# Optimization experiments

Measured on AMD Instinct MI355X. Metric: run time of the kernel, lower is better.

## Reference

```python
import jax, jax.numpy as jnp
import numpy as np

B, SEQ, PRED, DM = 16, 2048, 2048, 64
P = SEQ + PRED            # PointNum = 4096, per-node feature length
NLAYER, HID = 3, 4096     # MLPNums, ggdmodel hidden sizes
NH, HS = 16, 4096         # NumAttentionHeads, HiddenSize
G_CONST, K = 1.0, 8
NN = DM * DM              # 4096 == P, MHSA input dim (required by original code)


def setup_inputs() -> dict:
    key = jax.random.key(0)
    ks = jax.random.split(key, 11)
    s_mlp = 1.0 / np.sqrt(P).astype(np.float32)
    s_att = 1.0 / np.sqrt(NN).astype(np.float32)
    s_out = 1.0 / np.sqrt(HS).astype(np.float32)
    return {
        "x": jax.random.normal(ks[0], (B, P, DM), jnp.float32),
        "W_mlp": jax.random.normal(ks[1], (NLAYER, P, HID), jnp.float32) * s_mlp,
        "b_mlp": jnp.zeros((NLAYER, HID), jnp.float32),
        "Wq": jax.random.normal(ks[2], (NN, HS), jnp.float32) * s_att,
        "bq": jnp.zeros((HS,), jnp.float32),
        "Wk": jax.random.normal(ks[3], (NN, HS), jnp.float32) * s_att,
        "bk": jnp.zeros((HS,), jnp.float32),
        "Wv": jax.random.normal(ks[4], (NN, HS), jnp.float32) * s_att,
        "bv": jnp.zeros((HS,), jnp.float32),
        "Wo": jax.random.normal(ks[5], (HS, HS), jnp.float32) * s_out,
        "bo": jnp.zeros((HS,), jnp.float32),
    }


def _grav_adj(h):
    # h: [B, N, D] node features -> symmetrized, top-K masked gravity adjacency [B, N, N]
    norm = jnp.linalg.norm(h, axis=-1)                      # [B, N]
    m = jnp.sum(h, axis=-1) / norm                          # node "mass"
    sim = jnp.einsum('bnd,bmd->bnm', h, h) / (norm[:, :, None] * norm[:, None, :])
    F = G_CONST * m[:, :, None] * m[:, None, :] * sim * sim  # gravity matrix
    kth = jax.lax.top_k(F, K)[0][..., -1:]                  # per-row Kth largest value
    F = jnp.where(F >= kth, F, 0.0)                         # keep only top-K per row
    F = jnp.maximum(F, 0.0)                                 # ReLU
    return 0.5 * (F + jnp.swapaxes(F, -1, -2))              # symmetrize


def reference(x, W_mlp, b_mlp, Wq, bq, Wk, bk, Wv, bv, Wo, bo):
    h = jnp.swapaxes(x, 1, 2)                               # [B, N=DM, P]
    adjs = [_grav_adj(h)]
    for l in range(NLAYER):                                 # each MLP applied to the same h
        hv = h @ W_mlp[l] + b_mlp[l]                        # [B, N, HID]
        adjs.append(_grav_adj(hv))
    A = jnp.stack(adjs, axis=1)                             # [B, L, N, N], L = NLAYER + 1
    Lseq = A.shape[1]
    tok = A.reshape(B, Lseq, NN)                            # L tokens of dim N*N
    dh = HS // NH
    q = (tok @ Wq + bq).reshape(B, Lseq, NH, dh)
    k = (tok @ Wk + bk).reshape(B, Lseq, NH, dh)
    v = (tok @ Wv + bv).reshape(B, Lseq, NH, dh)
    scores = jnp.einsum('blhd,bmhd->bhlm', q, k) / np.sqrt(dh).astype(np.float32)
    attn = jax.nn.softmax(scores, axis=-1)
    ctx = jnp.einsum('bhlm,bmhd->blhd', attn, v).reshape(B, Lseq, HS)
    out = ctx @ Wo + bo                                     # [B, L, HS]
    return jnp.where(out > 0.5, out, 0.0)
```

## Files before the change

### kernel.cpp

```cpp
#include <hip/hip_runtime.h>
#include <math.h>


#define B16 16
#define PDIM 4096
#define NNODE 64
#define NCHUNK 32
#define KCG 128

typedef __attribute__((ext_vector_type(8))) short bf16x8;
typedef __attribute__((ext_vector_type(4))) float f32x4;
typedef __attribute__((ext_vector_type(4))) unsigned short us4;
typedef __attribute__((ext_vector_type(8))) unsigned short us8;

__device__ inline void split2(float x, unsigned short& h, unsigned short& l) {
  unsigned u = __float_as_uint(x);
  unsigned hu = (u + 0x7fffu + ((u >> 16) & 1u)) & 0xffff0000u;
  h = (unsigned short)(hu >> 16);
  float lo = x - __uint_as_float(hu);
  unsigned u2 = __float_as_uint(lo);
  l = (unsigned short)((u2 + 0x7fffu + ((u2 >> 16) & 1u)) >> 16);
}

__device__ inline void gload16(const void* g, void* lds) {
  __builtin_amdgcn_global_load_lds((const unsigned int*)g, (unsigned int*)lds, 16, 0, 0);
}

__global__ __launch_bounds__(256) void k_transpose(const float* __restrict__ x,
                                                   float* __restrict__ h,
                                                   unsigned short* __restrict__ AhT,
                                                   unsigned short* __restrict__ AlT,
                                                   int do_split) {
  __shared__ float t[64][65];
  int b = blockIdx.y;
  int p0 = blockIdx.x * 64;
  const float* xb = x + (size_t)b * PDIM * NNODE;
  float* hb = h + (size_t)b * NNODE * PDIM;
#pragma unroll
  for (int i = 0; i < 16; ++i) {
    int e = i * 256 + threadIdx.x;
    int p = e >> 6, n = e & 63;
    t[p][n] = xb[(size_t)p0 * 64 + e];
  }
  __syncthreads();
#pragma unroll
  for (int i = 0; i < 16; ++i) {
    int e = i * 256 + threadIdx.x;
    int n = e >> 6, p = e & 63;
    hb[(size_t)n * PDIM + p0 + p] = t[p][n];
  }
  if (!do_split) return;
#pragma unroll
  for (int j = 0; j < 2; ++j) {
    int cid = j * 256 + threadIdx.x;
    int n2 = cid >> 3, kg8 = cid & 7;
    us8 hv_, lv_;
#pragma unroll
    for (int e = 0; e < 8; ++e) {
      unsigned short hh, ll;
      split2(t[kg8 * 8 + e][n2], hh, ll);
      hv_[e] = hh; lv_[e] = ll;
    }
    int m = b * 64 + n2;
    int ks = (p0 >> 5) + (kg8 >> 2);
    size_t idx = (((size_t)(m >> 7) * 128 + ks) * 8 + ((m >> 4) & 7)) * 512 +
                 (size_t)((n2 & 15) + 16 * (kg8 & 3)) * 8;
    *(us8*)&AhT[idx] = hv_;
    *(us8*)&AlT[idx] = lv_;
  }
}

__global__ __launch_bounds__(256) void k_wsplit(const float* __restrict__ W,
                                                unsigned short* __restrict__ WhT,
                                                unsigned short* __restrict__ WlT) {
  __shared__ float Wt[32][132];
  int nb = blockIdx.x, kb = blockIdx.y;
  int tid = threadIdx.x;
#pragma unroll
  for (int i = 0; i < 4; ++i) {
    int idx = i * 256 + tid;
    int row = idx >> 5, c4 = idx & 31;
    float4 v = *(const float4*)&W[(size_t)(kb * 32 + row) * 4096 + nb * 128 + c4 * 4];
    *(float4*)&Wt[row][c4 * 4] = v;
  }
  __syncthreads();
#pragma unroll
  for (int j = 0; j < 2; ++j) {
    int cid = j * 256 + tid;
    int nl = cid & 127, kg = cid >> 7;
    us8 hv_, lv_;
#pragma unroll
    for (int e = 0; e < 8; ++e) {
      unsigned short hh, ll;
      split2(Wt[kg * 8 + e][nl], hh, ll);
      hv_[e] = hh; lv_[e] = ll;
    }
    size_t idx = (((size_t)nb * 128 + kb) * 8 + (nl >> 4)) * 512 +
                 (size_t)((nl & 15) + 16 * kg) * 8;
    *(us8*)&WhT[idx] = hv_;
    *(us8*)&WlT[idx] = lv_;
  }
}

__global__ __launch_bounds__(512, 4) void k_gemm_bf16(
    const unsigned short* __restrict__ Ah, const unsigned short* __restrict__ Al,
    const unsigned short* __restrict__ Bh, const unsigned short* __restrict__ Bl,
    float* __restrict__ Cp, int Ksteps, int ksplit, int N, int mstore) {
  __shared__ unsigned short sAh[2][4096], sAl[2][4096];
  __shared__ unsigned short sBh[2][4096], sBl[2][4096];
  int tid = threadIdx.x;
  int l = tid & 63, wid = tid >> 6;
  int wr = wid >> 2, wc = wid & 3;
  int nb = blockIdx.x, mb = blockIdx.y, z = blockIdx.z;
  int spp = Ksteps / ksplit;
  int ks0 = z * spp;

  const size_t abase = ((size_t)mb * Ksteps + ks0) * 4096 + tid * 8;
  const size_t bbase = ((size_t)nb * Ksteps + ks0) * 4096 + tid * 8;

  f32x4 acc[4][2];
#pragma unroll
  for (int i = 0; i < 4; ++i)
#pragma unroll
    for (int j = 0; j < 2; ++j) acc[i][j] = (f32x4){0.f, 0.f, 0.f, 0.f};

  gload16(Ah + abase, &sAh[0][tid * 8]);
  gload16(Al + abase, &sAl[0][tid * 8]);
  gload16(Bh + bbase, &sBh[0][tid * 8]);
  gload16(Bl + bbase, &sBl[0][tid * 8]);
  __syncthreads();

  int buf = 0;
  for (int t = 0; t < spp; ++t) {
    if (t + 1 < spp) {
      size_t off = (size_t)(t + 1) * 4096;
      gload16(Ah + abase + off, &sAh[buf ^ 1][tid * 8]);
      gload16(Al + abase + off, &sAl[buf ^ 1][tid * 8]);
      gload16(Bh + bbase + off, &sBh[buf ^ 1][tid * 8]);
      gload16(Bl + bbase + off, &sBl[buf ^ 1][tid * 8]);
    }
    bf16x8 ah[4], al4[4], bh2[2], bl2[2];
#pragma unroll
    for (int mt = 0; mt < 4; ++mt) {
      ah[mt]  = *(const bf16x8*)&sAh[buf][(wr * 4 + mt) * 512 + l * 8];
      al4[mt] = *(const bf16x8*)&sAl[buf][(wr * 4 + mt) * 512 + l * 8];
    }
#pragma unroll
    for (int nt = 0; nt < 2; ++nt) {
      bh2[nt] = *(const bf16x8*)&sBh[buf][(wc * 2 + nt) * 512 + l * 8];
      bl2[nt] = *(const bf16x8*)&sBl[buf][(wc * 2 + nt) * 512 + l * 8];
    }
#pragma unroll
    for (int mt = 0; mt < 4; ++mt)
#pragma unroll
      for (int nt = 0; nt < 2; ++nt) {
        acc[mt][nt] = __builtin_amdgcn_mfma_f32_16x16x32_bf16(ah[mt],  bh2[nt], acc[mt][nt], 0, 0, 0);
        acc[mt][nt] = __builtin_amdgcn_mfma_f32_16x16x32_bf16(ah[mt],  bl2[nt], acc[mt][nt], 0, 0, 0);
        acc[mt][nt] = __builtin_amdgcn_mfma_f32_16x16x32_bf16(al4[mt], bh2[nt], acc[mt][nt], 0, 0, 0);
      }
    __syncthreads();
    buf ^= 1;
  }

  int n0 = nb * 128, m0 = mb * 128;
  float* Cz = Cp + (size_t)z * mstore * N;
#pragma unroll
  for (int mt = 0; mt < 4; ++mt)
#pragma unroll
    for (int nt = 0; nt < 2; ++nt) {
      int col = n0 + wc * 32 + nt * 16 + (l & 15);
#pragma unroll
      for (int r = 0; r < 4; ++r) {
        int row = m0 + wr * 64 + mt * 16 + ((l >> 4) << 2) + r;
        if (row < mstore) Cz[(size_t)row * N + col] = acc[mt][nt][r];
      }
    }
}

__global__ __launch_bounds__(256) void k_red_mlp(const float* __restrict__ Cp,
                                                 const float* __restrict__ bias,
                                                 float* __restrict__ hv) {
  int idx = blockIdx.x * 256 + threadIdx.x;
  hv[idx] = Cp[idx] + Cp[idx + 4194304] + bias[idx & 4095];
}

__global__ __launch_bounds__(256) void k_red16(const float* __restrict__ Cp,
                                               const float* __restrict__ bias,
                                               float* __restrict__ dst, int thr) {
  int idx = blockIdx.x * 256 + threadIdx.x;
  float s = bias[idx & 4095];
#pragma unroll
  for (int p = 0; p < 16; ++p) s += Cp[(size_t)p * 262144 + idx];
  if (thr) s = (s > 0.5f) ? s : 0.f;
  dst[idx] = s;
}

__global__ __launch_bounds__(256) void k_gram_partial(const float* __restrict__ Z,
                                                      float* __restrict__ Gp,
                                                      float* __restrict__ Sp) {
  __shared__ float Zt[KCG][68];
  int c = blockIdx.x, b = blockIdx.y;
  int tid = threadIdx.x;
  const float* Zb = Z + (size_t)b * NNODE * PDIM + c * KCG;
#pragma unroll
  for (int i = 0; i < 32; ++i) {
    int e = i * 256 + tid;
    int r = e >> 7, kk = e & 127;
    Zt[kk][r] = Zb[(size_t)r * PDIM + kk];
  }
  __syncthreads();
  int ii = tid >> 2, j0 = (tid & 3) << 4;
  float acc[16] = {};
  for (int kk = 0; kk < KCG; ++kk) {
    float zi = Zt[kk][ii];
    float4 z0 = *(const float4*)&Zt[kk][j0 + 0];
    float4 z1 = *(const float4*)&Zt[kk][j0 + 4];
    float4 z2 = *(const float4*)&Zt[kk][j0 + 8];
    float4 z3 = *(const float4*)&Zt[kk][j0 + 12];
    acc[0] = fmaf(zi, z0.x, acc[0]);   acc[1] = fmaf(zi, z0.y, acc[1]);
    acc[2] = fmaf(zi, z0.z, acc[2]);   acc[3] = fmaf(zi, z0.w, acc[3]);
    acc[4] = fmaf(zi, z1.x, acc[4]);   acc[5] = fmaf(zi, z1.y, acc[5]);
    acc[6] = fmaf(zi, z1.z, acc[6]);   acc[7] = fmaf(zi, z1.w, acc[7]);
    acc[8] = fmaf(zi, z2.x, acc[8]);   acc[9] = fmaf(zi, z2.y, acc[9]);
    acc[10] = fmaf(zi, z2.z, acc[10]); acc[11] = fmaf(zi, z2.w, acc[11]);
    acc[12] = fmaf(zi, z3.x, acc[12]); acc[13] = fmaf(zi, z3.y, acc[13]);
    acc[14] = fmaf(zi, z3.z, acc[14]); acc[15] = fmaf(zi, z3.w, acc[15]);
  }
  float* gp = Gp + ((size_t)c * B16 + b) * 4096 + ii * 64 + j0;
#pragma unroll
  for (int j = 0; j < 16; ++j) gp[j] = acc[j];
  if (tid < 64) {
    float s = 0.f;
    for (int kk = 0; kk < KCG; ++kk) s += Zt[kk][tid];
    Sp[((size_t)c * B16 + b) * 64 + tid] = s;
  }
}

__global__ __launch_bounds__(256) void k_gram_reduce(const float* __restrict__ Gp,
                                                     const float* __restrict__ Sp,
                                                     float* __restrict__ G,
                                                     float* __restrict__ S, int slot) {
  int idx = blockIdx.x * 256 + threadIdx.x;
  if (idx < B16 * 4096) {
    float s = 0.f;
    for (int c = 0; c < NCHUNK; ++c) s += Gp[(size_t)c * (B16 * 4096) + idx];
    G[(size_t)slot * (B16 * 4096) + idx] = s;
  } else {
    int idx2 = idx - B16 * 4096;
    float s = 0.f;
    for (int c = 0; c < NCHUNK; ++c) s += Sp[(size_t)c * (B16 * 64) + idx2];
    S[(size_t)slot * (B16 * 64) + idx2] = s;
  }
}

__device__ inline float wmax64(float v) {
#pragma unroll
  for (int off = 32; off; off >>= 1) v = fmaxf(v, __shfl_xor(v, off));
  return v;
}

__global__ __launch_bounds__(256) void k_adj_t(const float* __restrict__ G,
                                               const float* __restrict__ S,
                                               unsigned short* __restrict__ tokh,
                                               unsigned short* __restrict__ tokl) {
  __shared__ float Fm[64][64];
  __shared__ float nrm[64], mm[64];
  int b = blockIdx.x >> 2, lz = blockIdx.x & 3;
  int tid = threadIdx.x;
  int j = tid & 63, w = tid >> 6;
  const float* Gb = G + ((size_t)lz * B16 + b) * 4096;
  const float* Sb = S + ((size_t)lz * B16 + b) * 64;
  if (tid < 64) {
    float nj = sqrtf(Gb[tid * 64 + tid]);
    nrm[tid] = nj;
    mm[tid] = Sb[tid] / nj;
  }
  __syncthreads();
  for (int i = w; i < 64; i += 4) {
    float g = Gb[i * 64 + j];
    float sim = g / (nrm[i] * nrm[j]);
    Fm[i][j] = mm[i] * mm[j] * sim * sim;
  }
  __syncthreads();
  for (int i = w; i < 64; i += 4) {
    float f = Fm[i][j];
    int cnt = 0;
#pragma unroll
    for (int u4 = 0; u4 < 16; ++u4) {
      float4 q = *(const float4*)&Fm[i][u4 * 4];
      cnt += (q.x > f) + (q.y > f) + (q.z > f) + (q.w > f);
    }
    float cand = (cnt <= 7) ? f : INFINITY;
#pragma unroll
    for (int off = 32; off; off >>= 1) cand = fminf(cand, __shfl_xor(cand, off));
    float fm = (f >= cand) ? fmaxf(f, 0.f) : 0.f;
    Fm[i][j] = fm;
  }
  __syncthreads();
  int r = b * 4 + lz;
  int mt = r >> 4, rl = r & 15;
#pragma unroll
  for (int c = 0; c < 2; ++c) {
    int cid = tid * 2 + c;
    int jj0 = cid >> 3, g = cid & 7;
    us8 hv_, lv_;
#pragma unroll
    for (int e = 0; e < 8; ++e) {
      int kcol = g * 8 + e;
      float val = 0.5f * (Fm[jj0][kcol] + Fm[kcol][jj0]);
      unsigned short hh, ll;
      split2(val, hh, ll);
      hv_[e] = hh; lv_[e] = ll;
    }
    int ks = jj0 * 2 + (g >> 2);
    size_t idx = ((size_t)ks * 8 + mt) * 512 + (size_t)(rl + 16 * (g & 3)) * 8;
    *(us8*)&tokh[idx] = hv_;
    *(us8*)&tokl[idx] = lv_;
  }
}

__global__ __launch_bounds__(64) void k_attn_t(const float* __restrict__ q,
                                               const float* __restrict__ k,
                                               const float* __restrict__ v,
                                               unsigned short* __restrict__ ctxh,
                                               unsigned short* __restrict__ ctxl) {
  __shared__ float cb[4][256];
  int hd = blockIdx.x, b = blockIdx.y;
  int t = threadIdx.x;
  float qr[4][4], kr[4][4], vr[4][4];
#pragma unroll
  for (int l = 0; l < 4; ++l)
#pragma unroll
    for (int s = 0; s < 4; ++s) {
      size_t off = ((size_t)(b * 4 + l)) * 4096 + hd * 256 + t + s * 64;
      qr[l][s] = q[off]; kr[l][s] = k[off]; vr[l][s] = v[off];
    }
  float sc[4][4];
#pragma unroll
  for (int l = 0; l < 4; ++l)
#pragma unroll
    for (int m = 0; m < 4; ++m) {
      float p = 0.f;
#pragma unroll
      for (int s = 0; s < 4; ++s) p = fmaf(qr[l][s], kr[m][s], p);
#pragma unroll
      for (int off = 32; off; off >>= 1) p += __shfl_xor(p, off);
      sc[l][m] = p * (1.0f / 16.0f);
    }
  float at[4][4];
#pragma unroll
  for (int l = 0; l < 4; ++l) {
    float mx = fmaxf(fmaxf(sc[l][0], sc[l][1]), fmaxf(sc[l][2], sc[l][3]));
    float e0 = expf(sc[l][0] - mx), e1 = expf(sc[l][1] - mx);
    float e2 = expf(sc[l][2] - mx), e3 = expf(sc[l][3] - mx);
    float d = e0 + e1 + e2 + e3;
    at[l][0] = e0 / d; at[l][1] = e1 / d; at[l][2] = e2 / d; at[l][3] = e3 / d;
  }
#pragma unroll
  for (int l = 0; l < 4; ++l)
#pragma unroll
    for (int s = 0; s < 4; ++s) {
      float c = 0.f;
#pragma unroll
      for (int m = 0; m < 4; ++m) c = fmaf(at[l][m], vr[m][s], c);
      cb[l][s * 64 + t] = c;
    }
  __syncthreads();
  int lq = t >> 4, c16 = t & 15;
  int mt = b >> 2, rl = (b & 3) * 4 + lq;
#pragma unroll
  for (int e8 = 0; e8 < 2; ++e8) {
    us8 hv_, lv_;
#pragma unroll
    for (int e = 0; e < 8; ++e) {
      unsigned short hh, ll;
      split2(cb[lq][c16 * 16 + e8 * 8 + e], hh, ll);
      hv_[e] = hh; lv_[e] = ll;
    }
    int ks = hd * 8 + (c16 >> 1);
    size_t idx = ((size_t)ks * 8 + mt) * 512 + (size_t)(rl + 16 * ((c16 * 2 + e8) & 3)) * 8;
    *(us8*)&ctxh[idx] = hv_;
    *(us8*)&ctxl[idx] = lv_;
  }
}

__global__ __launch_bounds__(256) void k_gemm_mfma(
    const float* __restrict__ A, const float* __restrict__ B0,
    const float* __restrict__ B1, const float* __restrict__ B2,
    const float* __restrict__ bias, float* __restrict__ C,
    int mrows, int mstore, int N, int K, int ksplit) {
  __shared__ __align__(16) unsigned short sA[2][8][64][8];
  __shared__ __align__(16) unsigned short sB[2][8][64][8];
  int z = blockIdx.z;
  int mat = z / ksplit, ks = z - mat * ksplit;
  const float* Bm = (mat == 0) ? B0 : ((mat == 1) ? B1 : B2);
  int kchunk = K / ksplit;
  int k0 = ks * kchunk, k1 = k0 + kchunk;
  int tid = threadIdx.x;
  int l = tid & 63;
  int wr = (tid >> 7) & 1, wc = (tid >> 6) & 1;
  int m0 = blockIdx.y * 128, n0g = blockIdx.x * 128;
  bool activeM = (m0 + wr * 64) < mstore;
  int am = tid >> 1;
  int arow = m0 + am; if (arow >= mrows) arow = mrows - 1;
  const float* Arow = A + (size_t)arow * K;
  int amt = am >> 4;
  int bk = tid >> 3;
  int bnb = (tid & 7) * 4;
  int bg = bk >> 3, bslot = bk & 7;
  f32x4 acc[4][4];
#pragma unroll
  for (int i = 0; i < 4; ++i)
#pragma unroll
    for (int j = 0; j < 4; ++j) acc[i][j] = (f32x4){0.f, 0.f, 0.f, 0.f};
  for (int kb = k0; kb < k1; kb += 32) {
    __syncthreads();
#pragma unroll
    for (int i = 0; i < 4; ++i) {
      int kq = (tid & 1) * 4 + i * 8;
      float4 a = *(const float4*)(Arow + kb + kq);
      unsigned short h0, h1, h2, h3, l0, l1, l2, l3;
      split2(a.x, h0, l0); split2(a.y, h1, l1);
      split2(a.z, h2, l2); split2(a.w, h3, l3);
      int lane_t = (am & 15) + 16 * (kq >> 3);
      int sb = kq & 4;
      *(us4*)&sA[0][amt][lane_t][sb] = (us4){h0, h1, h2, h3};
      *(us4*)&sA[1][amt][lane_t][sb] = (us4){l0, l1, l2, l3};
    }
    {
      const float* Brow = Bm + (size_t)(kb + bk) * N + n0g;
#pragma unroll
      for (int i = 0; i < 4; ++i) {
        int n = bnb + i * 32;
        int nt = n >> 4, nr = n & 15;
        float4 b = *(const float4*)(Brow + n);
        float be[4] = {b.x, b.y, b.z, b.w};
#pragma unroll
        for (int e = 0; e < 4; ++e) {
          unsigned short hh, ll;
          split2(be[e], hh, ll);
          sB[0][nt][nr + e + 16 * bg][bslot] = hh;
          sB[1][nt][nr + e + 16 * bg][bslot] = ll;
        }
      }
    }
    __syncthreads();
    if (!activeM) continue;
    bf16x8 ah[4], al[4], bh[4], bl[4];
#pragma unroll
    for (int t = 0; t < 4; ++t) {
      ah[t] = *(const bf16x8*)&sA[0][wr * 4 + t][l][0];
      al[t] = *(const bf16x8*)&sA[1][wr * 4 + t][l][0];
      bh[t] = *(const bf16x8*)&sB[0][wc * 4 + t][l][0];
      bl[t] = *(const bf16x8*)&sB[1][wc * 4 + t][l][0];
    }
#pragma unroll
    for (int mt = 0; mt < 4; ++mt)
#pragma unroll
      for (int nt = 0; nt < 4; ++nt) {
        acc[mt][nt] = __builtin_amdgcn_mfma_f32_16x16x32_bf16(ah[mt], bh[nt], acc[mt][nt], 0, 0, 0);
        acc[mt][nt] = __builtin_amdgcn_mfma_f32_16x16x32_bf16(ah[mt], bl[nt], acc[mt][nt], 0, 0, 0);
        acc[mt][nt] = __builtin_amdgcn_mfma_f32_16x16x32_bf16(al[mt], bh[nt], acc[mt][nt], 0, 0, 0);
      }
  }
  if (!activeM) return;
  float* Cz = C + (size_t)z * mstore * N;
#pragma unroll
  for (int mt = 0; mt < 4; ++mt)
#pragma unroll
    for (int nt = 0; nt < 4; ++nt) {
      int col = n0g + wc * 64 + nt * 16 + (l & 15);
      float badd = bias ? bias[col] : 0.f;
#pragma unroll
      for (int r = 0; r < 4; ++r) {
        int row = m0 + wr * 64 + mt * 16 + ((l >> 4) << 2) + r;
        if (row < mstore) Cz[(size_t)row * N + col] = acc[mt][nt][r] + badd;
      }
    }
}

__global__ __launch_bounds__(64) void k_adj_fb(const float* __restrict__ G,
                                               const float* __restrict__ S,
                                               float* __restrict__ tok) {
  __shared__ float Fm[64][64];
  __shared__ float nrm[64], mm[64];
  int b = blockIdx.x >> 2, lz = blockIdx.x & 3;
  int j = threadIdx.x;
  const float* Gb = G + ((size_t)lz * B16 + b) * 4096;
  const float* Sb = S + ((size_t)lz * B16 + b) * 64;
  float nj = sqrtf(Gb[j * 64 + j]);
  nrm[j] = nj;
  mm[j] = Sb[j] / nj;
  __syncthreads();
  float mj = mm[j];
  for (int i = 0; i < 64; ++i) {
    float g = Gb[i * 64 + j];
    float sim = g / (nrm[i] * nj);
    float F = mm[i] * mj * sim * sim;
    float v = F;
    bool act = true;
    float kth = 0.f;
#pragma unroll
    for (int it = 0; it < 8; ++it) {
      float mv = wmax64(act ? v : -INFINITY);
      kth = mv;
      unsigned long long ball = __ballot(act && (v == mv));
      int first = __ffsll(ball) - 1;
      if (j == first) act = false;
    }
    float fm = (F >= kth) ? F : 0.f;
    Fm[i][j] = fmaxf(fm, 0.f);
  }
  __syncthreads();
  float* tb = tok + ((size_t)b * 4 + lz) * 4096;
  for (int i = 0; i < 64; ++i) tb[i * 64 + j] = 0.5f * (Fm[i][j] + Fm[j][i]);
}

__global__ __launch_bounds__(256) void k_qkv_reduce(const float* __restrict__ Cp,
                                                    const float* __restrict__ bq,
                                                    const float* __restrict__ bk,
                                                    const float* __restrict__ bv,
                                                    float* __restrict__ q,
                                                    float* __restrict__ k,
                                                    float* __restrict__ v) {
  int idx = blockIdx.x * 256 + threadIdx.x;
  int mat = idx >> 18;
  int rn = idx & ((1 << 18) - 1);
  int n = rn & 4095;
  const float* base = Cp + (size_t)mat * 4 * 262144;
  float s = base[rn] + base[rn + 262144] + base[rn + 2 * 262144] + base[rn + 3 * 262144];
  if (mat == 0) q[rn] = s + bq[n];
  else if (mat == 1) k[rn] = s + bk[n];
  else v[rn] = s + bv[n];
}

__global__ __launch_bounds__(64) void k_attn_fb(const float* __restrict__ q,
                                                const float* __restrict__ k,
                                                const float* __restrict__ v,
                                                float* __restrict__ ctx) {
  int hd = blockIdx.x, b = blockIdx.y;
  int t = threadIdx.x;
  float qr[4][4], kr[4][4], vr[4][4];
#pragma unroll
  for (int l = 0; l < 4; ++l)
#pragma unroll
    for (int s = 0; s < 4; ++s) {
      size_t off = ((size_t)(b * 4 + l)) * 4096 + hd * 256 + t + s * 64;
      qr[l][s] = q[off]; kr[l][s] = k[off]; vr[l][s] = v[off];
    }
  float sc[4][4];
#pragma unroll
  for (int l = 0; l < 4; ++l)
#pragma unroll
    for (int m = 0; m < 4; ++m) {
      float p = 0.f;
#pragma unroll
      for (int s = 0; s < 4; ++s) p = fmaf(qr[l][s], kr[m][s], p);
#pragma unroll
      for (int off = 32; off; off >>= 1) p += __shfl_xor(p, off);
      sc[l][m] = p * (1.0f / 16.0f);
    }
  float at[4][4];
#pragma unroll
  for (int l = 0; l < 4; ++l) {
    float mx = fmaxf(fmaxf(sc[l][0], sc[l][1]), fmaxf(sc[l][2], sc[l][3]));
    float e0 = expf(sc[l][0] - mx), e1 = expf(sc[l][1] - mx);
    float e2 = expf(sc[l][2] - mx), e3 = expf(sc[l][3] - mx);
    float d = e0 + e1 + e2 + e3;
    at[l][0] = e0 / d; at[l][1] = e1 / d; at[l][2] = e2 / d; at[l][3] = e3 / d;
  }
#pragma unroll
  for (int l = 0; l < 4; ++l)
#pragma unroll
    for (int s = 0; s < 4; ++s) {
      float c = 0.f;
#pragma unroll
      for (int m = 0; m < 4; ++m) c = fmaf(at[l][m], vr[m][s], c);
      ctx[((size_t)(b * 4 + l)) * 4096 + hd * 256 + t + s * 64] = c;
    }
}

__global__ __launch_bounds__(256) void k_out_reduce(const float* __restrict__ Cp,
                                                    const float* __restrict__ bo,
                                                    float* __restrict__ out) {
  int idx = blockIdx.x * 256 + threadIdx.x;
  int n = idx & 4095;
  float s = bo[n];
#pragma unroll
  for (int p = 0; p < 8; ++p) s += Cp[(size_t)p * 262144 + idx];
  out[idx] = (s > 0.5f) ? s : 0.f;
}

extern "C" void kernel_launch(void* const* d_in, const int* in_sizes, int n_in,
                              void* d_out, int out_size, void* d_ws, size_t ws_size,
                              hipStream_t stream) {
  const float* x     = (const float*)d_in[0];
  const float* W_mlp = (const float*)d_in[1];
  const float* b_mlp = (const float*)d_in[2];
  const float* Wq = (const float*)d_in[3]; const float* bq = (const float*)d_in[4];
  const float* Wk = (const float*)d_in[5]; const float* bk = (const float*)d_in[6];
  const float* Wv = (const float*)d_in[7]; const float* bv = (const float*)d_in[8];
  const float* Wo = (const float*)d_in[9]; const float* bo = (const float*)d_in[10];
  float* out = (float*)d_out;
  float* ws = (float*)d_ws;

  float* h   = ws;
  float* hv  = ws + 4194304;
  float* Gp  = ws + 8388608;
  float* Sp  = ws + 10485760;
  float* G   = ws + 10518528;
  float* S   = ws + 10780672;

  const size_t NEED = 41979904ull * 4ull;
  if (ws_size >= NEED) {
    float* q   = ws + 10784768;
    float* kk  = ws + 11046912;
    float* vv  = ws + 11309056;
    unsigned short* AhT = (unsigned short*)(ws + 11571200);
    unsigned short* AlT = (unsigned short*)(ws + 13668352);
    unsigned short* WhT = (unsigned short*)(ws + 15765504);
    unsigned short* WlT = (unsigned short*)(ws + 24154112);
    float* Cp           = ws + 32542720;
    unsigned short* tokh = (unsigned short*)(ws + 40931328);
    unsigned short* tokl = (unsigned short*)(ws + 41193472);
    unsigned short* ctxh = (unsigned short*)(ws + 41455616);
    unsigned short* ctxl = (unsigned short*)(ws + 41717760);

    k_transpose<<<dim3(64, 16), 256, 0, stream>>>(x, h, AhT, AlT, 1);

    k_gram_partial<<<dim3(NCHUNK, 16), 256, 0, stream>>>(h, Gp, Sp);
    k_gram_reduce<<<260, 256, 0, stream>>>(Gp, Sp, G, S, 0);

    for (int l = 0; l < 3; ++l) {
      k_wsplit<<<dim3(32, 128), 256, 0, stream>>>(W_mlp + (size_t)l * 16777216, WhT, WlT);
      k_gemm_bf16<<<dim3(32, 8, 2), 512, 0, stream>>>(AhT, AlT, WhT, WlT, Cp,
                                                      128, 2, 4096, 1024);
      k_red_mlp<<<16384, 256, 0, stream>>>(Cp, b_mlp + (size_t)l * 4096, hv);
      k_gram_partial<<<dim3(NCHUNK, 16), 256, 0, stream>>>(hv, Gp, Sp);
      k_gram_reduce<<<260, 256, 0, stream>>>(Gp, Sp, G, S, l + 1);
    }

    hipMemsetAsync(tokh, 0, 4194304, stream);
    k_adj_t<<<64, 256, 0, stream>>>(G, S, tokh, tokl);

    const float* Wsrc[3] = {Wq, Wk, Wv};
    const float* bsrc[3] = {bq, bk, bv};
    float* dsts[3] = {q, kk, vv};
    for (int m = 0; m < 3; ++m) {
      k_wsplit<<<dim3(32, 128), 256, 0, stream>>>(Wsrc[m], WhT, WlT);
      k_gemm_bf16<<<dim3(32, 1, 16), 512, 0, stream>>>(tokh, tokl, WhT, WlT, Cp,
                                                       128, 16, 4096, 64);
      k_red16<<<1024, 256, 0, stream>>>(Cp, bsrc[m], dsts[m], 0);
    }

    k_attn_t<<<dim3(16, 16), 64, 0, stream>>>(q, kk, vv, ctxh, ctxl);

    k_wsplit<<<dim3(32, 128), 256, 0, stream>>>(Wo, WhT, WlT);
    k_gemm_bf16<<<dim3(32, 1, 16), 512, 0, stream>>>(ctxh, ctxl, WhT, WlT, Cp,
                                                     128, 16, 4096, 64);
    k_red16<<<1024, 256, 0, stream>>>(Cp, bo, out, 1);
  } else {
    float* tok = ws + 10784768;
    float* q   = ws + 11046912;
    float* kk  = ws + 11309056;
    float* vv  = ws + 11571200;
    float* ctx = ws + 11833344;
    float* qkvp = hv;
    float* op   = h;

    k_transpose<<<dim3(64, 16), 256, 0, stream>>>(x, h, (unsigned short*)0,
                                                  (unsigned short*)0, 0);
    k_gram_partial<<<dim3(NCHUNK, 16), 256, 0, stream>>>(h, Gp, Sp);
    k_gram_reduce<<<260, 256, 0, stream>>>(Gp, Sp, G, S, 0);
    for (int l = 0; l < 3; ++l) {
      const float* Wl = W_mlp + (size_t)l * PDIM * 4096;
      const float* bl = b_mlp + (size_t)l * 4096;
      k_gemm_mfma<<<dim3(32, 8, 1), 256, 0, stream>>>(h, Wl, Wl, Wl, bl, hv,
                                                      1024, 1024, 4096, 4096, 1);
      k_gram_partial<<<dim3(NCHUNK, 16), 256, 0, stream>>>(hv, Gp, Sp);
      k_gram_reduce<<<260, 256, 0, stream>>>(Gp, Sp, G, S, l + 1);
    }
    k_adj_fb<<<64, 64, 0, stream>>>(G, S, tok);
    k_gemm_mfma<<<dim3(32, 1, 12), 256, 0, stream>>>(tok, Wq, Wk, Wv, nullptr, qkvp,
                                                     64, 64, 4096, 4096, 4);
    k_qkv_reduce<<<3072, 256, 0, stream>>>(qkvp, bq, bk, bv, q, kk, vv);
    k_attn_fb<<<dim3(16, 16), 64, 0, stream>>>(q, kk, vv, ctx);
    k_gemm_mfma<<<dim3(32, 1, 8), 256, 0, stream>>>(ctx, Wo, Wo, Wo, nullptr, op,
                                                    64, 64, 4096, 4096, 8);
    k_out_reduce<<<1024, 256, 0, stream>>>(op, bo, out);
  }
}
```

Measured before the change: 641.7 us.

## Fuse weight split into skinny GEMMs and move Gram matrices onto MFMA

The QKV and output projections now read fp32 weights directly and do the hi/lo bf16 split inside the GEMM tile loader. This removes the separate k_wsplit passes and their intermediate weight buffers, and Q/K/V are batched into one launch. The Gram/row-sum computation becomes an MFMA kernel over pre-split bf16 operands, with the MLP bias reduction emitting that split layout directly. The fp32 transpose write and the token memset are also dropped. The trade-off is redundant split work per tile and a smaller 64-row tile with less reuse.

```diff
diff --git a/kernel.cpp b/kernel.cpp
--- a/kernel.cpp
+++ b/kernel.cpp
@@ -30,12 +30,11 @@
                                                    float* __restrict__ h,
                                                    unsigned short* __restrict__ AhT,
                                                    unsigned short* __restrict__ AlT,
-                                                   int do_split) {
+                                                   int mode) {
   __shared__ float t[64][65];
   int b = blockIdx.y;
   int p0 = blockIdx.x * 64;
   const float* xb = x + (size_t)b * PDIM * NNODE;
-  float* hb = h + (size_t)b * NNODE * PDIM;
 #pragma unroll
   for (int i = 0; i < 16; ++i) {
     int e = i * 256 + threadIdx.x;
@@ -43,13 +42,16 @@
     t[p][n] = xb[(size_t)p0 * 64 + e];
   }
   __syncthreads();
-#pragma unroll
-  for (int i = 0; i < 16; ++i) {
-    int e = i * 256 + threadIdx.x;
-    int n = e >> 6, p = e & 63;
-    hb[(size_t)n * PDIM + p0 + p] = t[p][n];
-  }
-  if (!do_split) return;
+  if (mode != 2) {
+    float* hb = h + (size_t)b * NNODE * PDIM;
+#pragma unroll
+    for (int i = 0; i < 16; ++i) {
+      int e = i * 256 + threadIdx.x;
+      int n = e >> 6, p = e & 63;
+      hb[(size_t)n * PDIM + p0 + p] = t[p][n];
+    }
+  }
+  if (mode == 0) return;
 #pragma unroll
   for (int j = 0; j < 2; ++j) {
     int cid = j * 256 + threadIdx.x;
@@ -177,22 +179,350 @@
     }
 }
 
-__global__ __launch_bounds__(256) void k_red_mlp(const float* __restrict__ Cp,
-                                                 const float* __restrict__ bias,
-                                                 float* __restrict__ hv) {
+__global__ __launch_bounds__(512) void k_gemm_wsf32(
+    const unsigned short* __restrict__ Ah, const unsigned short* __restrict__ Al,
+    const float* __restrict__ W0, const float* __restrict__ W1,
+    const float* __restrict__ W2, float* __restrict__ Cp, int ksplit) {
+  __shared__ unsigned short sAh[2][2048], sAl[2][2048];
+  __shared__ unsigned short sBh[2][4096], sBl[2][4096];
+  int tid = threadIdx.x;
+  int l = tid & 63, wid = tid >> 6;
+  int wr = wid >> 1, wc = wid & 1;
+  wr = wid >> 2; wc = wid & 3;
+  int nb = blockIdx.x, z = blockIdx.z;
+  int mat = z / ksplit, kz = z - mat * ksplit;
+  const float* W = (mat == 0) ? W0 : ((mat == 1) ? W1 : W2);
+  int nsteps = 128 / ksplit;
+  int ks0 = kz * nsteps;
+  int n0 = nb * 128;
+
+  int c0 = tid * 2;
+  f32x4 acc[2][2];
+#pragma unroll
+  for (int i = 0; i < 2; ++i)
+#pragma unroll
+    for (int j = 0; j < 2; ++j) acc[i][j] = (f32x4){0.f, 0.f, 0.f, 0.f};
+
+  {
+    int ks = ks0;
+    if (tid < 256) gload16(Ah + (size_t)ks * 4096 + tid * 8, &sAh[0][tid * 8]);
+    else           gload16(Al + (size_t)ks * 4096 + (tid - 256) * 8, &sAl[0][(tid - 256) * 8]);
+#pragma unroll
+    for (int cc = 0; cc < 2; ++cc) {
+      int c = c0 + cc;
+      int k = c >> 5, n = (c & 31) * 4;
+      float4 wv = *(const float4*)&W[(size_t)(ks * 32 + k) * 4096 + n0 + n];
+      int nt = n >> 4, lane = (n & 15) + 16 * (k >> 3), slot = k & 7;
+      unsigned short hh, ll;
+      split2(wv.x, hh, ll); sBh[0][nt*512+(lane+0)*8+slot] = hh; sBl[0][nt*512+(lane+0)*8+slot] = ll;
+      split2(wv.y, hh, ll); sBh[0][nt*512+(lane+1)*8+slot] = hh; sBl[0][nt*512+(lane+1)*8+slot] = ll;
+      split2(wv.z, hh, ll); sBh[0][nt*512+(lane+2)*8+slot] = hh; sBl[0][nt*512+(lane+2)*8+slot] = ll;
+      split2(wv.w, hh, ll); sBh[0][nt*512+(lane+3)*8+slot] = hh; sBl[0][nt*512+(lane+3)*8+slot] = ll;
+    }
+  }
+  __syncthreads();
+
+  int buf = 0;
+  for (int t = 0; t < nsteps; ++t) {
+    if (t + 1 < nsteps) {
+      int ks = ks0 + t + 1;
+      if (tid < 256) gload16(Ah + (size_t)ks * 4096 + tid * 8, &sAh[buf ^ 1][tid * 8]);
+      else           gload16(Al + (size_t)ks * 4096 + (tid - 256) * 8, &sAl[buf ^ 1][(tid - 256) * 8]);
+#pragma unroll
+      for (int cc = 0; cc < 2; ++cc) {
+        int c = c0 + cc;
+        int k = c >> 5, n = (c & 31) * 4;
+        float4 wv = *(const float4*)&W[(size_t)(ks * 32 + k) * 4096 + n0 + n];
+        int nt = n >> 4, lane = (n & 15) + 16 * (k >> 3), slot = k & 7;
+        unsigned short hh, ll;
+        split2(wv.x, hh, ll); sBh[buf^1][nt*512+(lane+0)*8+slot] = hh; sBl[buf^1][nt*512+(lane+0)*8+slot] = ll;
+        split2(wv.y, hh, ll); sBh[buf^1][nt*512+(lane+1)*8+slot] = hh; sBl[buf^1][nt*512+(lane+1)*8+slot] = ll;
+        split2(wv.z, hh, ll); sBh[buf^1][nt*512+(lane+2)*8+slot] = hh; sBl[buf^1][nt*512+(lane+2)*8+slot] = ll;
+        split2(wv.w, hh, ll); sBh[buf^1][nt*512+(lane+3)*8+slot] = hh; sBl[buf^1][nt*512+(lane+3)*8+slot] = ll;
+      }
+    }
+    bf16x8 aH[2], aL[2], bH[2], bL[2];
+#pragma unroll
+    for (int i = 0; i < 2; ++i) {
+      aH[i] = *(const bf16x8*)&sAh[buf][(wr * 2 + i) * 512 + l * 8];
+      aL[i] = *(const bf16x8*)&sAl[buf][(wr * 2 + i) * 512 + l * 8];
+      bH[i] = *(const bf16x8*)&sBh[buf][(wc * 2 + i) * 512 + l * 8];
+      bL[i] = *(const bf16x8*)&sBl[buf][(wc * 2 + i) * 512 + l * 8];
+    }
+#pragma unroll
+    for (int i = 0; i < 2; ++i)
+#pragma unroll
+      for (int j = 0; j < 2; ++j) {
+        acc[i][j] = __builtin_amdgcn_mfma_f32_16x16x32_bf16(aH[i], bH[j], acc[i][j], 0, 0, 0);
+        acc[i][j] = __builtin_amdgcn_mfma_f32_16x16x32_bf16(aH[i], bL[j], acc[i][j], 0, 0, 0);
+        acc[i][j] = __builtin_amdgcn_mfma_f32_16x16x32_bf16(aL[i], bH[j], acc[i][j], 0, 0, 0);
+      }
+    __syncthreads();
+    buf ^= 1;
+  }
+
+  float* Cz = Cp + (size_t)z * 262144;
+#pragma unroll
+  for (int i = 0; i < 2; ++i)
+#pragma unroll
+    for (int j = 0; j < 2; ++j) {
+      int col = n0 + wc * 32 + j * 16 + (l & 15);
+#pragma unroll
+      for (int r = 0; r < 4; ++r) {
+        int row = (wr * 2 + i) * 16 + ((l >> 4) << 2) + r;
+        Cz[(size_t)row * 4096 + col] = acc[i][j][r];
+      }
+    }
+}
+
+__global__ __launch_bounds__(256) void k_red_mlp_split(const float* __restrict__ Cp,
+                                                       const float* __restrict__ bias,
+                                                       unsigned short* __restrict__ hvh,
+                                                       unsigned short* __restrict__ hvl) {
+  int c = blockIdx.x * 256 + threadIdx.x;
+  int m = c >> 9, kc = c & 511;
+  int k0 = kc * 8;
+  const float* p = Cp + (size_t)m * 4096 + k0;
+  us8 hv_, lv_;
+#pragma unroll
+  for (int e = 0; e < 8; ++e) {
+    float v = p[e] + p[e + 4194304] + bias[k0 + e];
+    unsigned short hh, ll;
+    split2(v, hh, ll);
+    hv_[e] = hh; lv_[e] = ll;
+  }
+  int batch = m >> 6, rr = m & 63;
+  size_t idx = (size_t)batch * 262144 + (size_t)(kc >> 2) * 2048 +
+               (size_t)(rr >> 4) * 512 + (size_t)((rr & 15) + 16 * (kc & 3)) * 8;
+  *(us8*)&hvh[idx] = hv_;
+  *(us8*)&hvl[idx] = lv_;
+}
+
+__global__ __launch_bounds__(256) void k_gram_mfma(
+    const unsigned short* __restrict__ Zh, const unsigned short* __restrict__ Zl,
+    float* __restrict__ Gp, float* __restrict__ Sp,
+    int bs1, int ks_stride, int nsteps) {
+  __shared__ unsigned short sZh[2][2048], sZl[2][2048];
+  int z = blockIdx.x, b = blockIdx.y;
+  int tid = threadIdx.x;
+  int l = tid & 63, w = tid >> 6;
+  size_t zbase = (size_t)(b >> 1) * 524288 + (size_t)(b & 1) * bs1;
+  int ks0 = z * nsteps;
+
+  f32x4 acc[4], racc;
+#pragma unroll
+  for (int j = 0; j < 4; ++j) acc[j] = (f32x4){0.f, 0.f, 0.f, 0.f};
+  racc = (f32x4){0.f, 0.f, 0.f, 0.f};
+  bf16x8 ones;
+#pragma unroll
+  for (int e = 0; e < 8; ++e) ones[e] = (short)0x3F80;
+
+  gload16(Zh + zbase + (size_t)ks0 * ks_stride + tid * 8, &sZh[0][tid * 8]);
+  gload16(Zl + zbase + (size_t)ks0 * ks_stride + tid * 8, &sZl[0][tid * 8]);
+  __syncthreads();
+
+  int buf = 0;
+  for (int t = 0; t < nsteps; ++t) {
+    if (t + 1 < nsteps) {
+      size_t off = zbase + (size_t)(ks0 + t + 1) * ks_stride + tid * 8;
+      gload16(Zh + off, &sZh[buf ^ 1][tid * 8]);
+      gload16(Zl + off, &sZl[buf ^ 1][tid * 8]);
+    }
+    bf16x8 bh[4], bl4[4];
+#pragma unroll
+    for (int nt = 0; nt < 4; ++nt) {
+      bh[nt]  = *(const bf16x8*)&sZh[buf][nt * 512 + l * 8];
+      bl4[nt] = *(const bf16x8*)&sZl[buf][nt * 512 + l * 8];
+    }
+    bf16x8 ah = bh[w], al = bl4[w];
+#pragma unroll
+    for (int nt = 0; nt < 4; ++nt) {
+      acc[nt] = __builtin_amdgcn_mfma_f32_16x16x32_bf16(ah, bh[nt], acc[nt], 0, 0, 0);
+      acc[nt] = __builtin_amdgcn_mfma_f32_16x16x32_bf16(ah, bl4[nt], acc[nt], 0, 0, 0);
+      acc[nt] = __builtin_amdgcn_mfma_f32_16x16x32_bf16(al, bh[nt], acc[nt], 0, 0, 0);
+    }
+    racc = __builtin_amdgcn_mfma_f32_16x16x32_bf16(ah, ones, racc, 0, 0, 0);
+    racc = __builtin_amdgcn_mfma_f32_16x16x32_bf16(al, ones, racc, 0, 0, 0);
+    __syncthreads();
+    buf ^= 1;
+  }
+
+  float* Gz = Gp + ((size_t)z * B16 + b) * 4096;
+#pragma unroll
+  for (int nt = 0; nt < 4; ++nt) {
+    int col = nt * 16 + (l & 15);
+#pragma unroll
+    for (int r = 0; r < 4; ++r) {
+      int row = w * 16 + ((l >> 4) << 2) + r;
+      Gz[row * 64 + col] = acc[nt][r];
+    }
+  }
+  if ((l & 15) == 0) {
+    float* Sz = Sp + ((size_t)z * B16 + b) * 64;
+#pragma unroll
+    for (int r = 0; r < 4; ++r) Sz[w * 16 + ((l >> 4) << 2) + r] = racc[r];
+  }
+}
+
+__global__ __launch_bounds__(256) void k_gred8(const float* __restrict__ Gp,
+                                               const float* __restrict__ Sp,
+                                               float* __restrict__ G,
+                                               float* __restrict__ S, int slot) {
   int idx = blockIdx.x * 256 + threadIdx.x;
-  hv[idx] = Cp[idx] + Cp[idx + 4194304] + bias[idx & 4095];
-}
-
-__global__ __launch_bounds__(256) void k_red16(const float* __restrict__ Cp,
-                                               const float* __restrict__ bias,
-                                               float* __restrict__ dst, int thr) {
+  if (idx < 65536) {
+    float s = 0.f;
+#pragma unroll
+    for (int c = 0; c < 8; ++c) s += Gp[(size_t)c * 65536 + idx];
+    G[(size_t)slot * 65536 + idx] = s;
+  } else if (idx < 66560) {
+    int i2 = idx - 65536;
+    float s = 0.f;
+#pragma unroll
+    for (int c = 0; c < 8; ++c) s += Sp[(size_t)c * 1024 + i2];
+    S[(size_t)slot * 1024 + i2] = s;
+  }
+}
+
+__global__ __launch_bounds__(256) void k_redN(const float* __restrict__ Cp,
+                                              const float* __restrict__ bias,
+                                              float* __restrict__ dst,
+                                              int nparts, int thr) {
   int idx = blockIdx.x * 256 + threadIdx.x;
   float s = bias[idx & 4095];
-#pragma unroll
-  for (int p = 0; p < 16; ++p) s += Cp[(size_t)p * 262144 + idx];
+  for (int p = 0; p < nparts; ++p) s += Cp[(size_t)p * 262144 + idx];
   if (thr) s = (s > 0.5f) ? s : 0.f;
   dst[idx] = s;
+}
+
+__device__ inline float wmax64(float v) {
+#pragma unroll
+  for (int off = 32; off; off >>= 1) v = fmaxf(v, __shfl_xor(v, off));
+  return v;
+}
+
+__global__ __launch_bounds__(256) void k_adj_t(const float* __restrict__ G,
+                                               const float* __restrict__ S,
+                                               unsigned short* __restrict__ tokh,
+                                               unsigned short* __restrict__ tokl) {
+  __shared__ float Fm[64][64];
+  __shared__ float nrm[64], mm[64];
+  int b = blockIdx.x >> 2, lz = blockIdx.x & 3;
+  int tid = threadIdx.x;
+  int j = tid & 63, w = tid >> 6;
+  const float* Gb = G + ((size_t)lz * B16 + b) * 4096;
+  const float* Sb = S + ((size_t)lz * B16 + b) * 64;
+  if (tid < 64) {
+    float nj = sqrtf(Gb[tid * 64 + tid]);
+    nrm[tid] = nj;
+    mm[tid] = Sb[tid] / nj;
+  }
+  __syncthreads();
+  for (int i = w; i < 64; i += 4) {
+    float g = Gb[i * 64 + j];
+    float sim = g / (nrm[i] * nrm[j]);
+    Fm[i][j] = mm[i] * mm[j] * sim * sim;
+  }
+  __syncthreads();
+  for (int i = w; i < 64; i += 4) {
+    float f = Fm[i][j];
+    int cnt = 0;
+#pragma unroll
+    for (int u4 = 0; u4 < 16; ++u4) {
+      float4 q = *(const float4*)&Fm[i][u4 * 4];
+      cnt += (q.x > f) + (q.y > f) + (q.z > f) + (q.w > f);
+    }
+    float cand = (cnt <= 7) ? f : INFINITY;
+#pragma unroll
+    for (int off = 32; off; off >>= 1) cand = fminf(cand, __shfl_xor(cand, off));
+    float fm = (f >= cand) ? fmaxf(f, 0.f) : 0.f;
+    Fm[i][j] = fm;
+  }
+  __syncthreads();
+  int r = b * 4 + lz;
+  int mt = r >> 4, rl = r & 15;
+#pragma unroll
+  for (int c = 0; c < 2; ++c) {
+    int cid = tid * 2 + c;
+    int jj0 = cid >> 3, g = cid & 7;
+    us8 hv_, lv_;
+#pragma unroll
+    for (int e = 0; e < 8; ++e) {
+      int kcol = g * 8 + e;
+      float val = 0.5f * (Fm[jj0][kcol] + Fm[kcol][jj0]);
+      unsigned short hh, ll;
+      split2(val, hh, ll);
+      hv_[e] = hh; lv_[e] = ll;
+    }
+    int ks = jj0 * 2 + (g >> 2);
+    size_t idx = ((size_t)ks * 8 + mt) * 512 + (size_t)(rl + 16 * (g & 3)) * 8;
+    *(us8*)&tokh[idx] = hv_;
+    *(us8*)&tokl[idx] = lv_;
+  }
+}
+
+__global__ __launch_bounds__(64) void k_attn_t(const float* __restrict__ q,
+                                               const float* __restrict__ k,
+                                               const float* __restrict__ v,
+                                               unsigned short* __restrict__ ctxh,
+                                               unsigned short* __restrict__ ctxl) {
+  __shared__ float cb[4][256];
+  int hd = blockIdx.x, b = blockIdx.y;
+  int t = threadIdx.x;
+  float qr[4][4], kr[4][4], vr[4][4];
+#pragma unroll
+  for (int l = 0; l < 4; ++l)
+#pragma unroll
+    for (int s = 0; s < 4; ++s) {
+      size_t off = ((size_t)(b * 4 + l)) * 4096 + hd * 256 + t + s * 64;
+      qr[l][s] = q[off]; kr[l][s] = k[off]; vr[l][s] = v[off];
+    }
+  float sc[4][4];
+#pragma unroll
+  for (int l = 0; l < 4; ++l)
+#pragma unroll
+    for (int m = 0; m < 4; ++m) {
+      float p = 0.f;
+#pragma unroll
+      for (int s = 0; s < 4; ++s) p = fmaf(qr[l][s], kr[m][s], p);
+#pragma unroll
+      for (int off = 32; off; off >>= 1) p += __shfl_xor(p, off);
+      sc[l][m] = p * (1.0f / 16.0f);
+    }
+  float at[4][4];
+#pragma unroll
+  for (int l = 0; l < 4; ++l) {
+    float mx = fmaxf(fmaxf(sc[l][0], sc[l][1]), fmaxf(sc[l][2], sc[l][3]));
+    float e0 = expf(sc[l][0] - mx), e1 = expf(sc[l][1] - mx);
+    float e2 = expf(sc[l][2] - mx), e3 = expf(sc[l][3] - mx);
+    float d = e0 + e1 + e2 + e3;
+    at[l][0] = e0 / d; at[l][1] = e1 / d; at[l][2] = e2 / d; at[l][3] = e3 / d;
+  }
+#pragma unroll
+  for (int l = 0; l < 4; ++l)
+#pragma unroll
+    for (int s = 0; s < 4; ++s) {
+      float c = 0.f;
+#pragma unroll
+      for (int m = 0; m < 4; ++m) c = fmaf(at[l][m], vr[m][s], c);
+      cb[l][s * 64 + t] = c;
+    }
+  __syncthreads();
+  int lq = t >> 4, c16 = t & 15;
+  int mt = b >> 2, rl = (b & 3) * 4 + lq;
+#pragma unroll
+  for (int e8 = 0; e8 < 2; ++e8) {
+    us8 hv_, lv_;
+#pragma unroll
+    for (int e = 0; e < 8; ++e) {
+      unsigned short hh, ll;
+      split2(cb[lq][c16 * 16 + e8 * 8 + e], hh, ll);
+      hv_[e] = hh; lv_[e] = ll;
+    }
+    int ks = hd * 8 + (c16 >> 1);
+    size_t idx = ((size_t)ks * 8 + mt) * 512 + (size_t)(rl + 16 * ((c16 * 2 + e8) & 3)) * 8;
+    *(us8*)&ctxh[idx] = hv_;
+    *(us8*)&ctxl[idx] = lv_;
+  }
 }
 
 __global__ __launch_bounds__(256) void k_gram_partial(const float* __restrict__ Z,
@@ -250,137 +580,6 @@
     float s = 0.f;
     for (int c = 0; c < NCHUNK; ++c) s += Sp[(size_t)c * (B16 * 64) + idx2];
     S[(size_t)slot * (B16 * 64) + idx2] = s;
-  }
-}
-
-__device__ inline float wmax64(float v) {
-#pragma unroll
-  for (int off = 32; off; off >>= 1) v = fmaxf(v, __shfl_xor(v, off));
-  return v;
-}
-
-__global__ __launch_bounds__(256) void k_adj_t(const float* __restrict__ G,
-                                               const float* __restrict__ S,
-                                               unsigned short* __restrict__ tokh,
-                                               unsigned short* __restrict__ tokl) {
-  __shared__ float Fm[64][64];
-  __shared__ float nrm[64], mm[64];
-  int b = blockIdx.x >> 2, lz = blockIdx.x & 3;
-  int tid = threadIdx.x;
-  int j = tid & 63, w = tid >> 6;
-  const float* Gb = G + ((size_t)lz * B16 + b) * 4096;
-  const float* Sb = S + ((size_t)lz * B16 + b) * 64;
-  if (tid < 64) {
-    float nj = sqrtf(Gb[tid * 64 + tid]);
-    nrm[tid] = nj;
-    mm[tid] = Sb[tid] / nj;
-  }
-  __syncthreads();
-  for (int i = w; i < 64; i += 4) {
-    float g = Gb[i * 64 + j];
-    float sim = g / (nrm[i] * nrm[j]);
-    Fm[i][j] = mm[i] * mm[j] * sim * sim;
-  }
-  __syncthreads();
-  for (int i = w; i < 64; i += 4) {
-    float f = Fm[i][j];
-    int cnt = 0;
-#pragma unroll
-    for (int u4 = 0; u4 < 16; ++u4) {
-      float4 q = *(const float4*)&Fm[i][u4 * 4];
-      cnt += (q.x > f) + (q.y > f) + (q.z > f) + (q.w > f);
-    }
-    float cand = (cnt <= 7) ? f : INFINITY;
-#pragma unroll
-    for (int off = 32; off; off >>= 1) cand = fminf(cand, __shfl_xor(cand, off));
-    float fm = (f >= cand) ? fmaxf(f, 0.f) : 0.f;
-    Fm[i][j] = fm;
-  }
-  __syncthreads();
-  int r = b * 4 + lz;
-  int mt = r >> 4, rl = r & 15;
-#pragma unroll
-  for (int c = 0; c < 2; ++c) {
-    int cid = tid * 2 + c;
-    int jj0 = cid >> 3, g = cid & 7;
-    us8 hv_, lv_;
-#pragma unroll
-    for (int e = 0; e < 8; ++e) {
-      int kcol = g * 8 + e;
-      float val = 0.5f * (Fm[jj0][kcol] + Fm[kcol][jj0]);
-      unsigned short hh, ll;
-      split2(val, hh, ll);
-      hv_[e] = hh; lv_[e] = ll;
-    }
-    int ks = jj0 * 2 + (g >> 2);
-    size_t idx = ((size_t)ks * 8 + mt) * 512 + (size_t)(rl + 16 * (g & 3)) * 8;
-    *(us8*)&tokh[idx] = hv_;
-    *(us8*)&tokl[idx] = lv_;
-  }
-}
-
-__global__ __launch_bounds__(64) void k_attn_t(const float* __restrict__ q,
-                                               const float* __restrict__ k,
-                                               const float* __restrict__ v,
-                                               unsigned short* __restrict__ ctxh,
-                                               unsigned short* __restrict__ ctxl) {
-  __shared__ float cb[4][256];
-  int hd = blockIdx.x, b = blockIdx.y;
-  int t = threadIdx.x;
-  float qr[4][4], kr[4][4], vr[4][4];
-#pragma unroll
-  for (int l = 0; l < 4; ++l)
-#pragma unroll
-    for (int s = 0; s < 4; ++s) {
-      size_t off = ((size_t)(b * 4 + l)) * 4096 + hd * 256 + t + s * 64;
-      qr[l][s] = q[off]; kr[l][s] = k[off]; vr[l][s] = v[off];
-    }
-  float sc[4][4];
-#pragma unroll
-  for (int l = 0; l < 4; ++l)
-#pragma unroll
-    for (int m = 0; m < 4; ++m) {
-      float p = 0.f;
-#pragma unroll
-      for (int s = 0; s < 4; ++s) p = fmaf(qr[l][s], kr[m][s], p);
-#pragma unroll
-      for (int off = 32; off; off >>= 1) p += __shfl_xor(p, off);
-      sc[l][m] = p * (1.0f / 16.0f);
-    }
-  float at[4][4];
-#pragma unroll
-  for (int l = 0; l < 4; ++l) {
-    float mx = fmaxf(fmaxf(sc[l][0], sc[l][1]), fmaxf(sc[l][2], sc[l][3]));
-    float e0 = expf(sc[l][0] - mx), e1 = expf(sc[l][1] - mx);
-    float e2 = expf(sc[l][2] - mx), e3 = expf(sc[l][3] - mx);
-    float d = e0 + e1 + e2 + e3;
-    at[l][0] = e0 / d; at[l][1] = e1 / d; at[l][2] = e2 / d; at[l][3] = e3 / d;
-  }
-#pragma unroll
-  for (int l = 0; l < 4; ++l)
-#pragma unroll
-    for (int s = 0; s < 4; ++s) {
-      float c = 0.f;
-#pragma unroll
-      for (int m = 0; m < 4; ++m) c = fmaf(at[l][m], vr[m][s], c);
-      cb[l][s * 64 + t] = c;
-    }
-  __syncthreads();
-  int lq = t >> 4, c16 = t & 15;
-  int mt = b >> 2, rl = (b & 3) * 4 + lq;
-#pragma unroll
-  for (int e8 = 0; e8 < 2; ++e8) {
-    us8 hv_, lv_;
-#pragma unroll
-    for (int e = 0; e < 8; ++e) {
-      unsigned short hh, ll;
-      split2(cb[lq][c16 * 16 + e8 * 8 + e], hh, ll);
-      hv_[e] = hh; lv_[e] = ll;
-    }
-    int ks = hd * 8 + (c16 >> 1);
-    size_t idx = ((size_t)ks * 8 + mt) * 512 + (size_t)(rl + 16 * ((c16 * 2 + e8) & 3)) * 8;
-    *(us8*)&ctxh[idx] = hv_;
-    *(us8*)&ctxl[idx] = lv_;
   }
 }
 
@@ -492,11 +691,10 @@
   nrm[j] = nj;
   mm[j] = Sb[j] / nj;
   __syncthreads();
-  float mj = mm[j];
   for (int i = 0; i < 64; ++i) {
     float g = Gb[i * 64 + j];
     float sim = g / (nrm[i] * nj);
-    float F = mm[i] * mj * sim * sim;
+    float F = mm[i] * mm[j] * sim * sim;
     float v = F;
     bool act = true;
     float kth = 0.f;
@@ -605,7 +803,6 @@
   float* ws = (float*)d_ws;
 
   float* h   = ws;
-  float* hv  = ws + 4194304;
   float* Gp  = ws + 8388608;
   float* Sp  = ws + 10485760;
   float* G   = ws + 10518528;
@@ -613,6 +810,8 @@
 
   const size_t NEED = 41979904ull * 4ull;
   if (ws_size >= NEED) {
+    unsigned short* hvh = (unsigned short*)(ws + 4194304);
+    unsigned short* hvl = (unsigned short*)(ws + 6291456);
     float* q   = ws + 10784768;
     float* kk  = ws + 11046912;
     float* vv  = ws + 11309056;
@@ -626,40 +825,33 @@
     unsigned short* ctxh = (unsigned short*)(ws + 41455616);
     unsigned short* ctxl = (unsigned short*)(ws + 41717760);
 
-    k_transpose<<<dim3(64, 16), 256, 0, stream>>>(x, h, AhT, AlT, 1);
-
-    k_gram_partial<<<dim3(NCHUNK, 16), 256, 0, stream>>>(h, Gp, Sp);
-    k_gram_reduce<<<260, 256, 0, stream>>>(Gp, Sp, G, S, 0);
+    k_transpose<<<dim3(64, 16), 256, 0, stream>>>(x, h, AhT, AlT, 2);
+
+    k_gram_mfma<<<dim3(8, 16), 256, 0, stream>>>(AhT, AlT, Gp, Sp, 2048, 4096, 16);
+    k_gred8<<<260, 256, 0, stream>>>(Gp, Sp, G, S, 0);
 
     for (int l = 0; l < 3; ++l) {
       k_wsplit<<<dim3(32, 128), 256, 0, stream>>>(W_mlp + (size_t)l * 16777216, WhT, WlT);
       k_gemm_bf16<<<dim3(32, 8, 2), 512, 0, stream>>>(AhT, AlT, WhT, WlT, Cp,
                                                       128, 2, 4096, 1024);
-      k_red_mlp<<<16384, 256, 0, stream>>>(Cp, b_mlp + (size_t)l * 4096, hv);
-      k_gram_partial<<<dim3(NCHUNK, 16), 256, 0, stream>>>(hv, Gp, Sp);
-      k_gram_reduce<<<260, 256, 0, stream>>>(Gp, Sp, G, S, l + 1);
-    }
-
-    hipMemsetAsync(tokh, 0, 4194304, stream);
+      k_red_mlp_split<<<2048, 256, 0, stream>>>(Cp, b_mlp + (size_t)l * 4096, hvh, hvl);
+      k_gram_mfma<<<dim3(8, 16), 256, 0, stream>>>(hvh, hvl, Gp, Sp, 262144, 2048, 16);
+      k_gred8<<<260, 256, 0, stream>>>(Gp, Sp, G, S, l + 1);
+    }
+
     k_adj_t<<<64, 256, 0, stream>>>(G, S, tokh, tokl);
 
-    const float* Wsrc[3] = {Wq, Wk, Wv};
-    const float* bsrc[3] = {bq, bk, bv};
-    float* dsts[3] = {q, kk, vv};
-    for (int m = 0; m < 3; ++m) {
-      k_wsplit<<<dim3(32, 128), 256, 0, stream>>>(Wsrc[m], WhT, WlT);
-      k_gemm_bf16<<<dim3(32, 1, 16), 512, 0, stream>>>(tokh, tokl, WhT, WlT, Cp,
-                                                       128, 16, 4096, 64);
-      k_red16<<<1024, 256, 0, stream>>>(Cp, bsrc[m], dsts[m], 0);
-    }
+    k_gemm_wsf32<<<dim3(32, 1, 24), 512, 0, stream>>>(tokh, tokl, Wq, Wk, Wv, Cp, 8);
+    k_redN<<<1024, 256, 0, stream>>>(Cp,                bq, q,  8, 0);
+    k_redN<<<1024, 256, 0, stream>>>(Cp + 8 * 262144,   bk, kk, 8, 0);
+    k_redN<<<1024, 256, 0, stream>>>(Cp + 16 * 262144,  bv, vv, 8, 0);
 
     k_attn_t<<<dim3(16, 16), 64, 0, stream>>>(q, kk, vv, ctxh, ctxl);
 
-    k_wsplit<<<dim3(32, 128), 256, 0, stream>>>(Wo, WhT, WlT);
-    k_gemm_bf16<<<dim3(32, 1, 16), 512, 0, stream>>>(ctxh, ctxl, WhT, WlT, Cp,
-                                                     128, 16, 4096, 64);
-    k_red16<<<1024, 256, 0, stream>>>(Cp, bo, out, 1);
+    k_gemm_wsf32<<<dim3(32, 1, 8), 512, 0, stream>>>(ctxh, ctxl, Wo, Wo, Wo, Cp, 8);
+    k_redN<<<1024, 256, 0, stream>>>(Cp, bo, out, 8, 1);
   } else {
+    float* hv  = ws + 4194304;
     float* tok = ws + 10784768;
     float* q   = ws + 11046912;
     float* kk  = ws + 11309056;
```

New measurement: 720.6 us. 12.3% more time.
